# Kernel tuning notes

Hardware: AMD Instinct MI355X
Metric: run time of the kernel (lower is better)

The kernel has to match this reference:

```python
import jax, jax.numpy as jnp
import numpy as np

D = 1024      # d_model
H = 16        # nhead
DH = 64       # qkv_dim (per-head)
FF = 4096     # dim_feedforward
EPS = 1e-5


def layer_norm(x, g, b):
    mu = jnp.mean(x, axis=-1, keepdims=True)
    var = jnp.mean(jnp.square(x - mu), axis=-1, keepdims=True)
    return (x - mu) * jax.lax.rsqrt(var + EPS) * g + b


def setup_inputs() -> dict:
    key = jax.random.key(0)
    ks = jax.random.split(key, 17)
    s = 0.02
    inp = {
        "src": jax.random.normal(ks[0], (2, 2048, D), jnp.float32),
        "qw": jax.random.normal(ks[1], (H * DH, D), jnp.float32) * s,
        "qb": jnp.zeros((H * DH,), jnp.float32),
        "kw": jax.random.normal(ks[2], (H * DH, D), jnp.float32) * s,
        "kb": jnp.zeros((H * DH,), jnp.float32),
        "vw": jax.random.normal(ks[3], (H * DH, D), jnp.float32) * s,
        "vb": jnp.zeros((H * DH,), jnp.float32),
        "ow": jax.random.normal(ks[4], (D, H * DH), jnp.float32) * s,
        "ob": jnp.zeros((D,), jnp.float32),
        "w1": jax.random.normal(ks[5], (FF, D), jnp.float32) * s,
        "b1": jnp.zeros((FF,), jnp.float32),
        "w2": jax.random.normal(ks[6], (D, FF), jnp.float32) * s,
        "b2": jnp.zeros((D,), jnp.float32),
        "g1": jnp.ones((D,), jnp.float32),
        "beta1": jnp.zeros((D,), jnp.float32),
        "g2": jnp.ones((D,), jnp.float32),
        "beta2": jnp.zeros((D,), jnp.float32),
    }
    return inp


def _attn(x, qw, qb, kw, kb, vw, vb, ow, ob):
    B, S, _ = x.shape
    scale = 1.0 / np.sqrt(DH)
    # projections -> [B, H, S, DH]
    q = (x @ qw.T + qb).reshape(B, S, H, DH).transpose(0, 2, 1, 3)
    k = (x @ kw.T + kb).reshape(B, S, H, DH).transpose(0, 2, 1, 3)
    v = (x @ vw.T + vb).reshape(B, S, H, DH).transpose(0, 2, 1, 3)
    scores = jnp.einsum('bhsd,bhtd->bhst', q, k) * scale
    attn = jax.nn.softmax(scores, axis=-1)
    out = jnp.einsum('bhst,bhtd->bhsd', attn, v)  # [B,H,S,DH]
    out = out.transpose(0, 2, 1, 3).reshape(B, S, H * DH)
    return out @ ow.T + ob


def reference(src, qw, qb, kw, kb, vw, vb, ow, ob, w1, b1, w2, b2, g1, beta1, g2, beta2):
    x = src
    # post-LN (norm_first=False), dropout=0 (eval)
    x = layer_norm(x + _attn(x, qw, qb, kw, kb, vw, vb, ow, ob), g1, beta1)
    ff = jax.nn.relu(x @ w1.T + b1) @ w2.T + b2
    x = layer_norm(x + ff, g2, beta2)
    return x
```

## Files before the change

kernel.cpp:

```cpp
#include <hip/hip_runtime.h>

typedef unsigned short bf16_t;
typedef unsigned short u16x8 __attribute__((ext_vector_type(8)));
typedef unsigned short u16x4 __attribute__((ext_vector_type(4)));
typedef float f32x4 __attribute__((ext_vector_type(4)));

#define D_MODEL 1024
#define NHEAD 16
#define DHEAD 64
#define FF_DIM 4096
#define SEQ 2048
#define BATCH 2
#define LOG2E 1.44269504088896340736f
#define EXP2F(x) __builtin_amdgcn_exp2f(x)

#define GLOAD_LDS16(gp, lp)                                          \
  __builtin_amdgcn_global_load_lds(                                  \
      (const __attribute__((address_space(1))) void*)(gp),           \
      (__attribute__((address_space(3))) void*)(lp), 16, 0, 0)

static __device__ __forceinline__ float bf2f(bf16_t b) {
  union { unsigned u; float f; } x;
  x.u = ((unsigned)b) << 16;
  return x.f;
}
static __device__ __forceinline__ bf16_t f2bf(float f) {
  union { float f; unsigned u; } x;
  x.f = f;
  unsigned r = (x.u + 0x7fffu + ((x.u >> 16) & 1u)) >> 16;
  return (bf16_t)r;
}
static __device__ __forceinline__ int cvtpk(float lo, float hi) {
  int r;
  asm("v_cvt_pk_bf16_f32 %0, %1, %2" : "=v"(r) : "v"(lo), "v"(hi));
  return r;
}
static __device__ __forceinline__ f32x4 mfma16(u16x8 a, u16x8 b, f32x4 c) {
  return __builtin_amdgcn_mfma_f32_16x16x32_bf16(a, b, c, 0, 0, 0);
}
static __device__ __forceinline__ u16x8 load8_f32(const float* q) {
  const float4 v0 = *(const float4*)(q);
  const float4 v1 = *(const float4*)(q + 4);
  u16x8 r;
  r[0] = f2bf(v0.x); r[1] = f2bf(v0.y); r[2] = f2bf(v0.z); r[3] = f2bf(v0.w);
  r[4] = f2bf(v1.x); r[5] = f2bf(v1.y); r[6] = f2bf(v1.z); r[7] = f2bf(v1.w);
  return r;
}

__global__ __launch_bounds__(256) void cvt_all(
    const float* __restrict__ src, bf16_t* __restrict__ dsrc,
    const float* __restrict__ qw, const float* __restrict__ kw,
    const float* __restrict__ vw, const float* __restrict__ ow,
    bf16_t* __restrict__ wqkv, bf16_t* __restrict__ owb,
    const float* __restrict__ w1, bf16_t* __restrict__ w1b,
    const float* __restrict__ w2, bf16_t* __restrict__ w2b) {
  const int b = blockIdx.x;
  const float* s;
  bf16_t* d;
  long off;
  if (b < 2048) {
    s = src; d = dsrc; off = (long)b * 2048;
  } else if (b < 4096) {
    const int seg = (b - 2048) >> 9, r = (b - 2048) & 511;
    s = seg == 0 ? qw : seg == 1 ? kw : seg == 2 ? vw : ow;
    d = (seg == 3) ? owb : wqkv + (long)seg * 1048576;
    off = (long)r * 2048;
  } else if (b < 6144) {
    s = w1; d = w1b; off = (long)(b - 4096) * 2048;
  } else {
    s = w2; d = w2b; off = (long)(b - 6144) * 2048;
  }
  const long i = off + threadIdx.x * 8;
  *(u16x8*)(d + i) = load8_f32(s + i);
}

template <int SMODE>
__global__ __launch_bounds__(256) void gemm_lds(
    const bf16_t* __restrict__ A, const bf16_t* __restrict__ W,
    const float* __restrict__ bq_, const float* __restrict__ bk_,
    const float* __restrict__ bv_, bf16_t* __restrict__ C0,
    bf16_t* __restrict__ C1, bf16_t* __restrict__ C2,
    bf16_t* __restrict__ C3,
    int N, int Kseg, long lda, long ldw, int relu, float qscale,
    int gxs) {
  __shared__ bf16_t As[128 * 64];
  __shared__ bf16_t Bs[128 * 64];
  const int tid = threadIdx.x;
  const int lane = tid & 63;
  const int w = tid >> 6;
  const int wr = w >> 1, wc = w & 1;
  const int g = lane >> 4, c = lane & 15;

  const int per = (int)gridDim.x >> 3;
  const int gt = (blockIdx.x & 7) * per + (blockIdx.x >> 3);
  const int u = gt & 31;
  const int st = gt >> 5;
  const int sx = st % gxs;
  const int t2 = st / gxs;
  const int sy = t2 & 7;
  const int z = t2 >> 3;
  const long bm = (long)(sy * 4 + (u & 3)) * 128;
  const long bn = (long)(sx * 8 + (u >> 2)) * 128;
  const long koff = (long)z * Kseg;

  f32x4 acc[4][4];
#pragma unroll
  for (int i = 0; i < 4; ++i)
#pragma unroll
    for (int j = 0; j < 4; ++j) acc[i][j] = (f32x4){0.f, 0.f, 0.f, 0.f};

  const int ckey = c & 7;

  for (int k0 = 0; k0 < Kseg; k0 += 64) {
    __syncthreads();
#pragma unroll
    for (int ld = 0; ld < 4; ++ld) {
      const int ch = ld * 256 + tid;
      const int row = ch >> 3;
      const int cc = (ch & 7) ^ (row & 7);
      GLOAD_LDS16(A + (bm + row) * lda + koff + k0 + cc * 8,
                  As + (ld * 256 + w * 64) * 8);
    }
#pragma unroll
    for (int ld = 0; ld < 4; ++ld) {
      const int ch = ld * 256 + tid;
      const int row = ch >> 3;
      const int cc = (ch & 7) ^ (row & 7);
      GLOAD_LDS16(W + (bn + row) * ldw + koff + k0 + cc * 8,
                  Bs + (ld * 256 + w * 64) * 8);
    }
    __syncthreads();
#pragma unroll
    for (int kk = 0; kk < 2; ++kk) {
      u16x8 af[4], bfv[4];
#pragma unroll
      for (int i = 0; i < 4; ++i)
        af[i] = *(const u16x8*)(
            As + ((wr * 64 + i * 16 + c) * 8 + ((kk * 4 + g) ^ ckey)) * 8);
#pragma unroll
      for (int j = 0; j < 4; ++j)
        bfv[j] = *(const u16x8*)(
            Bs + ((wc * 64 + j * 16 + c) * 8 + ((kk * 4 + g) ^ ckey)) * 8);
      __builtin_amdgcn_s_setprio(1);
#pragma unroll
      for (int i = 0; i < 4; ++i)
#pragma unroll
        for (int j = 0; j < 4; ++j)
          acc[i][j] = mfma16(af[i], bfv[j], acc[i][j]);
      __builtin_amdgcn_s_setprio(0);
    }
  }

  bf16_t* __restrict__ pp =
      (z == 0) ? C0 : (z == 1) ? C1 : (z == 2) ? C2 : C3;
#pragma unroll
  for (int i = 0; i < 4; ++i) {
#pragma unroll
    for (int j = 0; j < 4; ++j) {
      const int nn = (int)bn + wc * 64 + j * 16 + c;
#pragma unroll
      for (int r = 0; r < 4; ++r) {
        const int mm = (int)bm + wr * 64 + i * 16 + g * 4 + r;
        if (SMODE == 0) {
          float v = acc[i][j][r] + bq_[nn];
          if (relu) v = fmaxf(v, 0.f);
          C0[(long)mm * N + nn] = f2bf(v);
        } else if (SMODE == 4) {
          pp[(long)mm * N + nn] = f2bf(acc[i][j][r]);
        } else {
          const int seg = nn >> 10;
          const int col = nn & 1023;
          const int h = col >> 6, dh = col & 63;
          const int b = mm >> 11, s = mm & 2047;
          if (seg == 0) {
            const float v = (acc[i][j][r] + bq_[col]) * qscale;
            C0[((((long)b * NHEAD + h) * SEQ + s) << 6) + dh] = f2bf(v);
          } else if (seg == 1) {
            const float v = acc[i][j][r] + bk_[col];
            C1[((((long)b * NHEAD + h) * SEQ + s) << 6) + dh] = f2bf(v);
          } else {
            const float v = acc[i][j][r] + bv_[col];
            C2[(((long)b * NHEAD + h) * DHEAD + dh) * SEQ + s] = f2bf(v);
          }
        }
      }
    }
  }
}

template <int KEY>
static __device__ __forceinline__ void stage_tile(
    const bf16_t* __restrict__ gbase, long rstride, bf16_t* lds,
    int tid, int w) {
#pragma unroll
  for (int i = 0; i < 2; ++i) {
    const int row = i * 32 + (tid >> 3);
    const int key = KEY ? ((row & 3) | ((row & 8) >> 1)) : (row & 7);
    const int c4 = (tid & 7) ^ key;
    GLOAD_LDS16(gbase + (long)row * rstride + c4 * 8,
                lds + (i * 256 + w * 64) * 8);
  }
}

__global__ __launch_bounds__(256, 2) void attn_fwd(
    const bf16_t* __restrict__ Q, const bf16_t* __restrict__ K,
    const bf16_t* __restrict__ Vt, bf16_t* __restrict__ O) {
  __shared__ bf16_t Ks0[64 * 64];
  __shared__ bf16_t Ks1[64 * 64];
  __shared__ bf16_t Vs0[64 * 64];
  __shared__ bf16_t Vs1[64 * 64];
  const int tid = threadIdx.x;
  const int lane = tid & 63;
  const int w = tid >> 6;
  const int g = lane >> 4, c = lane & 15;
  const int lb = blockIdx.x;
  const int xcd = lb & 7, sl = lb >> 3;
  const int bh = xcd * 4 + (sl >> 4);
  const int q0 = (sl & 15) * 128 + w * 32;
  const bf16_t* Qb = Q + (long)bh * SEQ * DHEAD;
  const bf16_t* Kb = K + (long)bh * SEQ * DHEAD;
  const bf16_t* Vb = Vt + (long)bh * DHEAD * SEQ;

  u16x8 bq[2][2];
#pragma unroll
  for (int qh = 0; qh < 2; ++qh) {
    bq[qh][0] = *(const u16x8*)(Qb + (q0 + qh * 16 + c) * DHEAD + g * 8);
    bq[qh][1] = *(const u16x8*)(Qb + (q0 + qh * 16 + c) * DHEAD + 32 + g * 8);
  }

  float m0 = -1e30f, m1 = -1e30f, lp0 = 0.f, lp1 = 0.f;
  f32x4 oacc[4][2];
#pragma unroll
  for (int d = 0; d < 4; ++d)
#pragma unroll
    for (int qh = 0; qh < 2; ++qh) oacc[d][qh] = (f32x4){0.f, 0.f, 0.f, 0.f};

  const int ck = c & 7;
  const int pr = ((c >> 2) << 3) | (c & 3);

  for (int t0 = 0; t0 < SEQ; t0 += 128) {
    __syncthreads();
    stage_tile<1>(Kb + (long)t0 * DHEAD, DHEAD, Ks0, tid, w);
    stage_tile<1>(Kb + (long)(t0 + 64) * DHEAD, DHEAD, Ks1, tid, w);
    stage_tile<0>(Vb + t0, SEQ, Vs0, tid, w);
    stage_tile<0>(Vb + t0 + 64, SEQ, Vs1, tid, w);
    __syncthreads();

#pragma unroll
    for (int sub = 0; sub < 2; ++sub) {
      const bf16_t* Ks = sub ? Ks1 : Ks0;
      const bf16_t* Vs = sub ? Vs1 : Vs0;

      f32x4 s[2][2][2];
#pragma unroll
      for (int tt = 0; tt < 2; ++tt) {
        const int rowA = (tt * 32 + pr) * 64;
        const int rowC = (tt * 32 + pr + 4) * 64;
        const u16x8 kA = *(const u16x8*)(Ks + rowA + (g ^ ck) * 8);
        const u16x8 kB = *(const u16x8*)(Ks + rowA + ((4 + g) ^ ck) * 8);
        const u16x8 kC = *(const u16x8*)(Ks + rowC + (g ^ ck) * 8);
        const u16x8 kD = *(const u16x8*)(Ks + rowC + ((4 + g) ^ ck) * 8);
        __builtin_amdgcn_s_setprio(1);
#pragma unroll
        for (int qh = 0; qh < 2; ++qh) {
          s[tt][0][qh] = mfma16(kA, bq[qh][0], (f32x4){0.f, 0.f, 0.f, 0.f});
          s[tt][0][qh] = mfma16(kB, bq[qh][1], s[tt][0][qh]);
          s[tt][1][qh] = mfma16(kC, bq[qh][0], (f32x4){0.f, 0.f, 0.f, 0.f});
          s[tt][1][qh] = mfma16(kD, bq[qh][1], s[tt][1][qh]);
        }
        __builtin_amdgcn_s_setprio(0);
      }

      float pmv[2];
#pragma unroll
      for (int qh = 0; qh < 2; ++qh) {
        float pm = s[0][0][qh][0];
#pragma unroll
        for (int tt = 0; tt < 2; ++tt)
#pragma unroll
          for (int pi = 0; pi < 2; ++pi)
#pragma unroll
            for (int r = 0; r < 4; ++r) pm = fmaxf(pm, s[tt][pi][qh][r]);
        pm = fmaxf(pm, __shfl_xor(pm, 16));
        pm = fmaxf(pm, __shfl_xor(pm, 32));
        pmv[qh] = pm;
      }
      if (!__all(pmv[0] <= m0 + 8.f && pmv[1] <= m1 + 8.f)) {
        const float mn0 = fmaxf(m0, pmv[0]);
        const float mn1 = fmaxf(m1, pmv[1]);
        const float f0 = EXP2F(m0 - mn0);
        const float f1 = EXP2F(m1 - mn1);
        m0 = mn0; m1 = mn1;
        lp0 *= f0; lp1 *= f1;
        float fb0[4], fb1[4];
#pragma unroll
        for (int r = 0; r < 4; ++r) {
          fb0[r] = __shfl(f0, 4 * g + r);
          fb1[r] = __shfl(f1, 4 * g + r);
        }
#pragma unroll
        for (int d = 0; d < 4; ++d)
#pragma unroll
          for (int r = 0; r < 4; ++r) {
            oacc[d][0][r] *= fb0[r];
            oacc[d][1][r] *= fb1[r];
          }
      }
      float ts0 = 0.f, ts1 = 0.f;
#pragma unroll
      for (int tt = 0; tt < 2; ++tt)
#pragma unroll
        for (int pi = 0; pi < 2; ++pi)
#pragma unroll
          for (int r = 0; r < 4; ++r) {
            s[tt][pi][0][r] = EXP2F(s[tt][pi][0][r] - m0);
            s[tt][pi][1][r] = EXP2F(s[tt][pi][1][r] - m1);
            ts0 += s[tt][pi][0][r];
            ts1 += s[tt][pi][1][r];
          }
      lp0 += ts0;
      lp1 += ts1;

      union { int u[4]; u16x8 v; } pu[2][2];
#pragma unroll
      for (int qh = 0; qh < 2; ++qh)
#pragma unroll
        for (int tt = 0; tt < 2; ++tt) {
          pu[qh][tt].u[0] = cvtpk(s[tt][0][qh][0], s[tt][0][qh][1]);
          pu[qh][tt].u[1] = cvtpk(s[tt][0][qh][2], s[tt][0][qh][3]);
          pu[qh][tt].u[2] = cvtpk(s[tt][1][qh][0], s[tt][1][qh][1]);
          pu[qh][tt].u[3] = cvtpk(s[tt][1][qh][2], s[tt][1][qh][3]);
        }

#pragma unroll
      for (int d = 0; d < 4; ++d) {
        const int rowb = (d * 16 + c) * 64;
        const u16x8 v0 = *(const u16x8*)(Vs + rowb + ((g ^ ck)) * 8);
        const u16x8 v1 = *(const u16x8*)(Vs + rowb + (((4 + g) ^ ck)) * 8);
        __builtin_amdgcn_s_setprio(1);
        oacc[d][0] = mfma16(pu[0][0].v, v0, oacc[d][0]);
        oacc[d][0] = mfma16(pu[0][1].v, v1, oacc[d][0]);
        oacc[d][1] = mfma16(pu[1][0].v, v0, oacc[d][1]);
        oacc[d][1] = mfma16(pu[1][1].v, v1, oacc[d][1]);
        __builtin_amdgcn_s_setprio(0);
      }
    }
  }

  const int b = bh >> 4, h = bh & 15;
#pragma unroll
  for (int qh = 0; qh < 2; ++qh) {
    float lt = qh ? lp1 : lp0;
    lt += __shfl_xor(lt, 16);
    lt += __shfl_xor(lt, 32);
#pragma unroll
    for (int r = 0; r < 4; ++r) {
      const float inv = 1.f / __shfl(lt, 4 * g + r);
      const long base =
          ((long)b * SEQ + q0 + qh * 16 + g * 4 + r) * D_MODEL + h * DHEAD;
#pragma unroll
      for (int d = 0; d < 4; ++d)
        O[base + d * 16 + c] = f2bf(oacc[d][qh][r] * inv);
    }
  }
}

template <int XF32, int OUTF32, int YPART>
__global__ __launch_bounds__(256) void add_ln(
    const void* __restrict__ X, const bf16_t* __restrict__ Y0,
    const bf16_t* __restrict__ Y1, const bf16_t* __restrict__ Y2,
    const bf16_t* __restrict__ Y3, const float* __restrict__ ybias,
    const float* __restrict__ gamma, const float* __restrict__ beta,
    void* __restrict__ Out) {
  __shared__ float red[2][4];
  const int tid = threadIdx.x;
  const int lane = tid & 63, w = tid >> 6;
  const long base = (long)blockIdx.x * D_MODEL;

  float xv[4];
  if (XF32) {
    const float4 t = *(const float4*)((const float*)X + base + tid * 4);
    xv[0] = t.x; xv[1] = t.y; xv[2] = t.z; xv[3] = t.w;
  } else {
    const u16x4 t = *(const u16x4*)((const bf16_t*)X + base + tid * 4);
#pragma unroll
    for (int i = 0; i < 4; ++i) xv[i] = bf2f(t[i]);
  }
  float yv[4];
  if (YPART) {
    const u16x4 t0 = *(const u16x4*)(Y0 + base + tid * 4);
    const u16x4 t1 = *(const u16x4*)(Y1 + base + tid * 4);
    const u16x4 t2 = *(const u16x4*)(Y2 + base + tid * 4);
    const u16x4 t3 = *(const u16x4*)(Y3 + base + tid * 4);
    const float4 bb = *(const float4*)(ybias + tid * 4);
#pragma unroll
    for (int i = 0; i < 4; ++i)
      yv[i] = ((bf2f(t0[i]) + bf2f(t1[i])) + (bf2f(t2[i]) + bf2f(t3[i]))) +
              ((const float*)&bb)[i];
  } else {
    const u16x4 t = *(const u16x4*)(Y0 + base + tid * 4);
#pragma unroll
    for (int i = 0; i < 4; ++i) yv[i] = bf2f(t[i]);
  }
  float v[4], s = 0.f, s2 = 0.f;
#pragma unroll
  for (int i = 0; i < 4; ++i) {
    const float t = xv[i] + yv[i];
    v[i] = t;
    s += t;
    s2 += t * t;
  }
#pragma unroll
  for (int off = 32; off; off >>= 1) {
    s += __shfl_xor(s, off);
    s2 += __shfl_xor(s2, off);
  }
  if (lane == 0) { red[0][w] = s; red[1][w] = s2; }
  __syncthreads();
  s = red[0][0] + red[0][1] + red[0][2] + red[0][3];
  s2 = red[1][0] + red[1][1] + red[1][2] + red[1][3];
  const float mu = s * (1.f / D_MODEL);
  const float var = s2 * (1.f / D_MODEL) - mu * mu;
  const float inv = rsqrtf(var + 1e-5f);
  const float4 gv = *(const float4*)(gamma + tid * 4);
  const float4 bv = *(const float4*)(beta + tid * 4);
  const float o0 = (v[0] - mu) * inv * gv.x + bv.x;
  const float o1 = (v[1] - mu) * inv * gv.y + bv.y;
  const float o2 = (v[2] - mu) * inv * gv.z + bv.z;
  const float o3 = (v[3] - mu) * inv * gv.w + bv.w;
  if (OUTF32) {
    float4 ov; ov.x = o0; ov.y = o1; ov.z = o2; ov.w = o3;
    *(float4*)((float*)Out + base + tid * 4) = ov;
  } else {
    u16x4 ov;
    ov[0] = f2bf(o0); ov[1] = f2bf(o1); ov[2] = f2bf(o2); ov[3] = f2bf(o3);
    *(u16x4*)((bf16_t*)Out + base + tid * 4) = ov;
  }
}

extern "C" void kernel_launch(void* const* d_in, const int* in_sizes, int n_in,
                              void* d_out, int out_size, void* d_ws, size_t ws_size,
                              hipStream_t stream) {
  const float* src = (const float*)d_in[0];
  const float* qw = (const float*)d_in[1];
  const float* qb = (const float*)d_in[2];
  const float* kw = (const float*)d_in[3];
  const float* kb = (const float*)d_in[4];
  const float* vw = (const float*)d_in[5];
  const float* vb = (const float*)d_in[6];
  const float* ow = (const float*)d_in[7];
  const float* ob = (const float*)d_in[8];
  const float* w1 = (const float*)d_in[9];
  const float* b1 = (const float*)d_in[10];
  const float* w2 = (const float*)d_in[11];
  const float* b2 = (const float*)d_in[12];
  const float* gam1 = (const float*)d_in[13];
  const float* bet1 = (const float*)d_in[14];
  const float* gam2 = (const float*)d_in[15];
  const float* bet2 = (const float*)d_in[16];

  char* ws = (char*)d_ws;
  const long MB = 1024 * 1024;
  bf16_t* Qw   = (bf16_t*)(ws + 0 * MB);
  bf16_t* Kw   = (bf16_t*)(ws + 8 * MB);
  bf16_t* Vt   = (bf16_t*)(ws + 16 * MB);
  bf16_t* A1   = (bf16_t*)(ws + 24 * MB);
  bf16_t* X1   = (bf16_t*)(ws + 40 * MB);
  bf16_t* srcB = (bf16_t*)(ws + 48 * MB);
  bf16_t* Wqkv = (bf16_t*)(ws + 56 * MB);
  bf16_t* OWb  = (bf16_t*)(ws + 62 * MB);
  bf16_t* W1b  = (bf16_t*)(ws + 64 * MB);
  bf16_t* W2b  = (bf16_t*)(ws + 72 * MB);
  bf16_t* Poa  = (bf16_t*)(ws + 0 * MB);
  bf16_t* Pob  = (bf16_t*)(ws + 8 * MB);
  bf16_t* Poc  = (bf16_t*)(ws + 16 * MB);
  bf16_t* Pod  = (bf16_t*)(ws + 48 * MB);
  bf16_t* F1   = (bf16_t*)(ws + 0 * MB);
  bf16_t* Pfa  = (bf16_t*)(ws + 48 * MB);
  bf16_t* Pfb  = (bf16_t*)(ws + 56 * MB);
  bf16_t* Pfc  = (bf16_t*)(ws + 64 * MB);
  bf16_t* Pfd  = (bf16_t*)(ws + 80 * MB);

  const int M = BATCH * SEQ;
  dim3 blk(256);
  const float qscale = 0.125f * LOG2E;

  cvt_all<<<dim3(8192), blk, 0, stream>>>(
      src, srcB, qw, kw, vw, ow, Wqkv, OWb, w1, W1b, w2, W2b);

  gemm_lds<3><<<dim3(768), blk, 0, stream>>>(
      srcB, Wqkv, qb, kb, vb, Qw, Kw, Vt, (bf16_t*)0,
      3072, 1024, 1024, 1024, 0, qscale, 3);
  attn_fwd<<<dim3(512), blk, 0, stream>>>(Qw, Kw, Vt, A1);
  gemm_lds<4><<<dim3(1024), blk, 0, stream>>>(
      A1, OWb, ob, ob, ob, Poa, Pob, Poc, Pod,
      1024, 256, 1024, 1024, 0, 1.f, 1);
  add_ln<1, 0, 1><<<dim3(M), blk, 0, stream>>>(
      src, Poa, Pob, Poc, Pod, ob, gam1, bet1, X1);
  gemm_lds<0><<<dim3(1024), blk, 0, stream>>>(
      X1, W1b, b1, b1, b1, F1, F1, F1, (bf16_t*)0,
      4096, 1024, 1024, 1024, 1, 1.f, 4);
  gemm_lds<4><<<dim3(1024), blk, 0, stream>>>(
      F1, W2b, b2, b2, b2, Pfa, Pfb, Pfc, Pfd,
      1024, 1024, 4096, 4096, 0, 1.f, 1);
  add_ln<0, 1, 1><<<dim3(M), blk, 0, stream>>>(
      X1, Pfa, Pfb, Pfc, Pfd, b2, gam2, bet2, d_out);
}
```

Measured before the change: 247.1 us.

## Shrink attention tile to 16 query rows per wave and double grid

The attention kernel now has each wave handle 16 query rows instead of 32, so a block covers 64 queries and the grid doubles to 1024 blocks. Launch bounds rise to 4 blocks per SM, which lowers per-thread register pressure and should raise occupancy and latency hiding. In exchange, every K/V tile staged into LDS is reused by half as many queries, doubling total K/V global and LDS traffic. The MFMA priority window also now spans the whole PV loop instead of each iteration.

```diff
diff --git a/kernel.cpp b/kernel.cpp
--- a/kernel.cpp
+++ b/kernel.cpp
@@ -202,7 +202,7 @@
   }
 }
 
-__global__ __launch_bounds__(256, 2) void attn_fwd(
+__global__ __launch_bounds__(256, 4) void attn_fwd(
     const bf16_t* __restrict__ Q, const bf16_t* __restrict__ K,
     const bf16_t* __restrict__ Vt, bf16_t* __restrict__ O) {
   __shared__ bf16_t Ks0[64 * 64];
@@ -215,25 +215,19 @@
   const int g = lane >> 4, c = lane & 15;
   const int lb = blockIdx.x;
   const int xcd = lb & 7, sl = lb >> 3;
-  const int bh = xcd * 4 + (sl >> 4);
-  const int q0 = (sl & 15) * 128 + w * 32;
+  const int bh = xcd * 4 + (sl >> 5);
+  const int q0 = (sl & 31) * 64 + w * 16;
   const bf16_t* Qb = Q + (long)bh * SEQ * DHEAD;
   const bf16_t* Kb = K + (long)bh * SEQ * DHEAD;
   const bf16_t* Vb = Vt + (long)bh * DHEAD * SEQ;
 
-  u16x8 bq[2][2];
-#pragma unroll
-  for (int qh = 0; qh < 2; ++qh) {
-    bq[qh][0] = *(const u16x8*)(Qb + (q0 + qh * 16 + c) * DHEAD + g * 8);
-    bq[qh][1] = *(const u16x8*)(Qb + (q0 + qh * 16 + c) * DHEAD + 32 + g * 8);
-  }
-
-  float m0 = -1e30f, m1 = -1e30f, lp0 = 0.f, lp1 = 0.f;
-  f32x4 oacc[4][2];
-#pragma unroll
-  for (int d = 0; d < 4; ++d)
-#pragma unroll
-    for (int qh = 0; qh < 2; ++qh) oacc[d][qh] = (f32x4){0.f, 0.f, 0.f, 0.f};
+  const u16x8 bq0 = *(const u16x8*)(Qb + (q0 + c) * DHEAD + g * 8);
+  const u16x8 bq1 = *(const u16x8*)(Qb + (q0 + c) * DHEAD + 32 + g * 8);
+
+  float m = -1e30f, lp = 0.f;
+  f32x4 oacc[4];
+#pragma unroll
+  for (int d = 0; d < 4; ++d) oacc[d] = (f32x4){0.f, 0.f, 0.f, 0.f};
 
   const int ck = c & 7;
   const int pr = ((c >> 2) << 3) | (c & 3);
@@ -251,7 +245,7 @@
       const bf16_t* Ks = sub ? Ks1 : Ks0;
       const bf16_t* Vs = sub ? Vs1 : Vs0;
 
-      f32x4 s[2][2][2];
+      f32x4 s[2][2];
 #pragma unroll
       for (int tt = 0; tt < 2; ++tt) {
         const int rowA = (tt * 32 + pr) * 64;
@@ -261,107 +255,79 @@
         const u16x8 kC = *(const u16x8*)(Ks + rowC + (g ^ ck) * 8);
         const u16x8 kD = *(const u16x8*)(Ks + rowC + ((4 + g) ^ ck) * 8);
         __builtin_amdgcn_s_setprio(1);
-#pragma unroll
-        for (int qh = 0; qh < 2; ++qh) {
-          s[tt][0][qh] = mfma16(kA, bq[qh][0], (f32x4){0.f, 0.f, 0.f, 0.f});
-          s[tt][0][qh] = mfma16(kB, bq[qh][1], s[tt][0][qh]);
-          s[tt][1][qh] = mfma16(kC, bq[qh][0], (f32x4){0.f, 0.f, 0.f, 0.f});
-          s[tt][1][qh] = mfma16(kD, bq[qh][1], s[tt][1][qh]);
-        }
+        s[tt][0] = mfma16(kA, bq0, (f32x4){0.f, 0.f, 0.f, 0.f});
+        s[tt][0] = mfma16(kB, bq1, s[tt][0]);
+        s[tt][1] = mfma16(kC, bq0, (f32x4){0.f, 0.f, 0.f, 0.f});
+        s[tt][1] = mfma16(kD, bq1, s[tt][1]);
         __builtin_amdgcn_s_setprio(0);
       }
 
-      float pmv[2];
-#pragma unroll
-      for (int qh = 0; qh < 2; ++qh) {
-        float pm = s[0][0][qh][0];
-#pragma unroll
-        for (int tt = 0; tt < 2; ++tt)
-#pragma unroll
-          for (int pi = 0; pi < 2; ++pi)
-#pragma unroll
-            for (int r = 0; r < 4; ++r) pm = fmaxf(pm, s[tt][pi][qh][r]);
-        pm = fmaxf(pm, __shfl_xor(pm, 16));
-        pm = fmaxf(pm, __shfl_xor(pm, 32));
-        pmv[qh] = pm;
+      float pm = s[0][0][0];
+#pragma unroll
+      for (int tt = 0; tt < 2; ++tt)
+#pragma unroll
+        for (int pi = 0; pi < 2; ++pi)
+#pragma unroll
+          for (int r = 0; r < 4; ++r) pm = fmaxf(pm, s[tt][pi][r]);
+      pm = fmaxf(pm, __shfl_xor(pm, 16));
+      pm = fmaxf(pm, __shfl_xor(pm, 32));
+      if (!__all(pm <= m + 8.f)) {
+        const float mn = fmaxf(m, pm);
+        const float f = EXP2F(m - mn);
+        m = mn;
+        lp *= f;
+        float fb[4];
+#pragma unroll
+        for (int r = 0; r < 4; ++r) fb[r] = __shfl(f, 4 * g + r);
+#pragma unroll
+        for (int d = 0; d < 4; ++d)
+#pragma unroll
+          for (int r = 0; r < 4; ++r) oacc[d][r] *= fb[r];
       }
-      if (!__all(pmv[0] <= m0 + 8.f && pmv[1] <= m1 + 8.f)) {
-        const float mn0 = fmaxf(m0, pmv[0]);
-        const float mn1 = fmaxf(m1, pmv[1]);
-        const float f0 = EXP2F(m0 - mn0);
-        const float f1 = EXP2F(m1 - mn1);
-        m0 = mn0; m1 = mn1;
-        lp0 *= f0; lp1 *= f1;
-        float fb0[4], fb1[4];
-#pragma unroll
-        for (int r = 0; r < 4; ++r) {
-          fb0[r] = __shfl(f0, 4 * g + r);
-          fb1[r] = __shfl(f1, 4 * g + r);
-        }
-#pragma unroll
-        for (int d = 0; d < 4; ++d)
+      float ts = 0.f;
+#pragma unroll
+      for (int tt = 0; tt < 2; ++tt)
+#pragma unroll
+        for (int pi = 0; pi < 2; ++pi)
 #pragma unroll
           for (int r = 0; r < 4; ++r) {
-            oacc[d][0][r] *= fb0[r];
-            oacc[d][1][r] *= fb1[r];
+            s[tt][pi][r] = EXP2F(s[tt][pi][r] - m);
+            ts += s[tt][pi][r];
           }
+      lp += ts;
+
+      union { int u[4]; u16x8 v; } pu[2];
+#pragma unroll
+      for (int tt = 0; tt < 2; ++tt) {
+        pu[tt].u[0] = cvtpk(s[tt][0][0], s[tt][0][1]);
+        pu[tt].u[1] = cvtpk(s[tt][0][2], s[tt][0][3]);
+        pu[tt].u[2] = cvtpk(s[tt][1][0], s[tt][1][1]);
+        pu[tt].u[3] = cvtpk(s[tt][1][2], s[tt][1][3]);
       }
-      float ts0 = 0.f, ts1 = 0.f;
-#pragma unroll
-      for (int tt = 0; tt < 2; ++tt)
-#pragma unroll
-        for (int pi = 0; pi < 2; ++pi)
-#pragma unroll
-          for (int r = 0; r < 4; ++r) {
-            s[tt][pi][0][r] = EXP2F(s[tt][pi][0][r] - m0);
-            s[tt][pi][1][r] = EXP2F(s[tt][pi][1][r] - m1);
-            ts0 += s[tt][pi][0][r];
-            ts1 += s[tt][pi][1][r];
-          }
-      lp0 += ts0;
-      lp1 += ts1;
-
-      union { int u[4]; u16x8 v; } pu[2][2];
-#pragma unroll
-      for (int qh = 0; qh < 2; ++qh)
-#pragma unroll
-        for (int tt = 0; tt < 2; ++tt) {
-          pu[qh][tt].u[0] = cvtpk(s[tt][0][qh][0], s[tt][0][qh][1]);
-          pu[qh][tt].u[1] = cvtpk(s[tt][0][qh][2], s[tt][0][qh][3]);
-          pu[qh][tt].u[2] = cvtpk(s[tt][1][qh][0], s[tt][1][qh][1]);
-          pu[qh][tt].u[3] = cvtpk(s[tt][1][qh][2], s[tt][1][qh][3]);
-        }
-
+
+      __builtin_amdgcn_s_setprio(1);
 #pragma unroll
       for (int d = 0; d < 4; ++d) {
         const int rowb = (d * 16 + c) * 64;
         const u16x8 v0 = *(const u16x8*)(Vs + rowb + ((g ^ ck)) * 8);
         const u16x8 v1 = *(const u16x8*)(Vs + rowb + (((4 + g) ^ ck)) * 8);
-        __builtin_amdgcn_s_setprio(1);
-        oacc[d][0] = mfma16(pu[0][0].v, v0, oacc[d][0]);
-        oacc[d][0] = mfma16(pu[0][1].v, v1, oacc[d][0]);
-        oacc[d][1] = mfma16(pu[1][0].v, v0, oacc[d][1]);
-        oacc[d][1] = mfma16(pu[1][1].v, v1, oacc[d][1]);
-        __builtin_amdgcn_s_setprio(0);
+        oacc[d] = mfma16(pu[0].v, v0, oacc[d]);
+        oacc[d] = mfma16(pu[1].v, v1, oacc[d]);
       }
+      __builtin_amdgcn_s_setprio(0);
     }
   }
 
+  float lt = lp;
+  lt += __shfl_xor(lt, 16);
+  lt += __shfl_xor(lt, 32);
   const int b = bh >> 4, h = bh & 15;
 #pragma unroll
-  for (int qh = 0; qh < 2; ++qh) {
-    float lt = qh ? lp1 : lp0;
-    lt += __shfl_xor(lt, 16);
-    lt += __shfl_xor(lt, 32);
-#pragma unroll
-    for (int r = 0; r < 4; ++r) {
-      const float inv = 1.f / __shfl(lt, 4 * g + r);
-      const long base =
-          ((long)b * SEQ + q0 + qh * 16 + g * 4 + r) * D_MODEL + h * DHEAD;
-#pragma unroll
-      for (int d = 0; d < 4; ++d)
-        O[base + d * 16 + c] = f2bf(oacc[d][qh][r] * inv);
-    }
+  for (int r = 0; r < 4; ++r) {
+    const float inv = 1.f / __shfl(lt, 4 * g + r);
+    const long base = ((long)b * SEQ + q0 + g * 4 + r) * D_MODEL + h * DHEAD;
+#pragma unroll
+    for (int d = 0; d < 4; ++d) O[base + d * 16 + c] = f2bf(oacc[d][r] * inv);
   }
 }
 
@@ -491,7 +457,7 @@
   gemm_lds<3><<<dim3(768), blk, 0, stream>>>(
       srcB, Wqkv, qb, kb, vb, Qw, Kw, Vt, (bf16_t*)0,
       3072, 1024, 1024, 1024, 0, qscale, 3);
-  attn_fwd<<<dim3(512), blk, 0, stream>>>(Qw, Kw, Vt, A1);
+  attn_fwd<<<dim3(1024), blk, 0, stream>>>(Qw, Kw, Vt, A1);
   gemm_lds<4><<<dim3(1024), blk, 0, stream>>>(
       A1, OWb, ob, ob, ob, Poa, Pob, Poc, Pod,
       1024, 256, 1024, 1024, 0, 1.f, 1);
```

Result: no change. 249.3 us (+0.9%).

## Double-buffer K/V tiles in attention to overlap loads with compute

Applied to the files above, without the earlier changes.

The attention kernel now keeps two sets of K/V shared-memory tiles. It prefetches the next 128-key block with direct global-to-LDS loads while the MFMA work runs on the current block, and uses one barrier per iteration instead of two. The aim is to hide global load latency and cut barrier stalls in the key loop. In exchange, LDS per block doubles to 64 KB. That still fits two blocks per CU, but it leaves little LDS headroom.

```diff
diff --git a/kernel.cpp b/kernel.cpp
--- a/kernel.cpp
+++ b/kernel.cpp
@@ -205,10 +205,8 @@
 __global__ __launch_bounds__(256, 2) void attn_fwd(
     const bf16_t* __restrict__ Q, const bf16_t* __restrict__ K,
     const bf16_t* __restrict__ Vt, bf16_t* __restrict__ O) {
-  __shared__ bf16_t Ks0[64 * 64];
-  __shared__ bf16_t Ks1[64 * 64];
-  __shared__ bf16_t Vs0[64 * 64];
-  __shared__ bf16_t Vs1[64 * 64];
+  __shared__ bf16_t Ks[2][2][64 * 64];
+  __shared__ bf16_t Vs[2][2][64 * 64];
   const int tid = threadIdx.x;
   const int lane = tid & 63;
   const int w = tid >> 6;
@@ -238,28 +236,37 @@
   const int ck = c & 7;
   const int pr = ((c >> 2) << 3) | (c & 3);
 
+  stage_tile<1>(Kb, DHEAD, Ks[0][0], tid, w);
+  stage_tile<1>(Kb + (long)64 * DHEAD, DHEAD, Ks[0][1], tid, w);
+  stage_tile<0>(Vb, SEQ, Vs[0][0], tid, w);
+  stage_tile<0>(Vb + 64, SEQ, Vs[0][1], tid, w);
+  __syncthreads();
+
+  int cur = 0;
   for (int t0 = 0; t0 < SEQ; t0 += 128) {
-    __syncthreads();
-    stage_tile<1>(Kb + (long)t0 * DHEAD, DHEAD, Ks0, tid, w);
-    stage_tile<1>(Kb + (long)(t0 + 64) * DHEAD, DHEAD, Ks1, tid, w);
-    stage_tile<0>(Vb + t0, SEQ, Vs0, tid, w);
-    stage_tile<0>(Vb + t0 + 64, SEQ, Vs1, tid, w);
-    __syncthreads();
+    if (t0 + 128 < SEQ) {
+      const int nb = cur ^ 1;
+      const long tn = t0 + 128;
+      stage_tile<1>(Kb + tn * DHEAD, DHEAD, Ks[nb][0], tid, w);
+      stage_tile<1>(Kb + (tn + 64) * DHEAD, DHEAD, Ks[nb][1], tid, w);
+      stage_tile<0>(Vb + tn, SEQ, Vs[nb][0], tid, w);
+      stage_tile<0>(Vb + tn + 64, SEQ, Vs[nb][1], tid, w);
+    }
 
 #pragma unroll
     for (int sub = 0; sub < 2; ++sub) {
-      const bf16_t* Ks = sub ? Ks1 : Ks0;
-      const bf16_t* Vs = sub ? Vs1 : Vs0;
+      const bf16_t* Ksb = Ks[cur][sub];
+      const bf16_t* Vsb = Vs[cur][sub];
 
       f32x4 s[2][2][2];
 #pragma unroll
       for (int tt = 0; tt < 2; ++tt) {
         const int rowA = (tt * 32 + pr) * 64;
         const int rowC = (tt * 32 + pr + 4) * 64;
-        const u16x8 kA = *(const u16x8*)(Ks + rowA + (g ^ ck) * 8);
-        const u16x8 kB = *(const u16x8*)(Ks + rowA + ((4 + g) ^ ck) * 8);
-        const u16x8 kC = *(const u16x8*)(Ks + rowC + (g ^ ck) * 8);
-        const u16x8 kD = *(const u16x8*)(Ks + rowC + ((4 + g) ^ ck) * 8);
+        const u16x8 kA = *(const u16x8*)(Ksb + rowA + (g ^ ck) * 8);
+        const u16x8 kB = *(const u16x8*)(Ksb + rowA + ((4 + g) ^ ck) * 8);
+        const u16x8 kC = *(const u16x8*)(Ksb + rowC + (g ^ ck) * 8);
+        const u16x8 kD = *(const u16x8*)(Ksb + rowC + ((4 + g) ^ ck) * 8);
         __builtin_amdgcn_s_setprio(1);
 #pragma unroll
         for (int qh = 0; qh < 2; ++qh) {
@@ -335,8 +342,8 @@
 #pragma unroll
       for (int d = 0; d < 4; ++d) {
         const int rowb = (d * 16 + c) * 64;
-        const u16x8 v0 = *(const u16x8*)(Vs + rowb + ((g ^ ck)) * 8);
-        const u16x8 v1 = *(const u16x8*)(Vs + rowb + (((4 + g) ^ ck)) * 8);
+        const u16x8 v0 = *(const u16x8*)(Vsb + rowb + ((g ^ ck)) * 8);
+        const u16x8 v1 = *(const u16x8*)(Vsb + rowb + (((4 + g) ^ ck)) * 8);
         __builtin_amdgcn_s_setprio(1);
         oacc[d][0] = mfma16(pu[0][0].v, v0, oacc[d][0]);
         oacc[d][0] = mfma16(pu[0][1].v, v1, oacc[d][0]);
@@ -345,6 +352,9 @@
         __builtin_amdgcn_s_setprio(0);
       }
     }
+
+    __syncthreads();
+    cur ^= 1;
   }
 
   const int b = bh >> 4, h = bh & 15;
```

Result: no change. 247.5 us (+0.2%).
